# Kernel optimization log

Measured on AMD Instinct MI355X. Metric: run time of the kernel, lower is better.

## Reference

```python
import jax, jax.numpy as jnp
from jax import lax
import numpy as np

NB_CODE = 16384
DIM = 128
SCALES = [(1, 1), (2, 2), (4, 4), (8, 8), (16, 16)]
PHI_IDX = [0, 1, 1, 2, 3]  # PhiPartiallyShared: argmin(|ticks - si/(SN-1)|), K=4, SN=5
RESI = 0.5  # abs(quant_resi)
BETA = 0.25


def _cubic(x, a=-0.75):
    # PyTorch bicubic kernel (cubic convolution, a=-0.75)
    ax = np.abs(x)
    return np.where(ax <= 1.0, (a + 2.0) * ax ** 3 - (a + 3.0) * ax ** 2 + 1.0,
                    np.where(ax < 2.0, a * ax ** 3 - 5.0 * a * ax ** 2 + 8.0 * a * ax - 4.0 * a, 0.0))


def bicubic_mat(n_in, n_out):
    # 1D interpolation matrix matching torch F.interpolate(mode='bicubic', align_corners=False)
    W = np.zeros((n_out, n_in), dtype=np.float32)
    scale = n_in / n_out
    for i in range(n_out):
        x = (i + 0.5) * scale - 0.5
        x0 = int(np.floor(x))
        t = x - x0
        for k in range(4):
            idx = min(max(x0 - 1 + k, 0), n_in - 1)  # border clamp
            W[i, idx] += _cubic(t + 1.0 - k)
    return jnp.asarray(W)


def phi_apply(h, w, b):
    y = lax.conv_general_dilated(h, w, (1, 1), 'SAME',
                                 dimension_numbers=('NCHW', 'OIHW', 'NCHW'))
    y = y + b[None, :, None, None]
    return h * (1.0 - RESI) + y * RESI


def setup_inputs() -> dict:
    key = jax.random.key(0)
    k1, k2, k3, k4 = jax.random.split(key, 4)
    B, C, J, L = 16, DIM, 16, 16
    f_bcjl = jax.random.normal(k1, (B, C, J, L), dtype=jnp.float32)
    emb = jax.random.normal(k2, (NB_CODE, C), dtype=jnp.float32) * 0.02
    # 4 partially-shared Phi convs (3x3, C->C)
    phi_w = jax.random.normal(k3, (4, C, C, 3, 3), dtype=jnp.float32) * (1.0 / np.sqrt(C * 9))
    phi_b = jax.random.normal(k4, (4, C), dtype=jnp.float32) * 0.01
    return {'f_bcjl': f_bcjl, 'emb': emb, 'phi_w': phi_w, 'phi_b': phi_b}


def reference(f_bcjl, emb, phi_w, phi_b):
    B, C, J, L = f_bcjl.shape
    SN = len(SCALES)
    f_ng = lax.stop_gradient(f_bcjl)
    f_rest = f_ng
    f_hat = jnp.zeros_like(f_ng)
    loss = jnp.float32(0.0)
    e_sq = jnp.sum(emb * emb, axis=1)  # [K]
    idx_all = []
    for si, (sn, tn) in enumerate(SCALES):
        if si != SN - 1:
            # 'area' downsample == integer-factor average pooling here
            r = f_rest.reshape(B, C, sn, J // sn, tn, L // tn).mean(axis=(3, 5))
        else:
            r = f_rest
        rNC = r.transpose(0, 2, 3, 1).reshape(-1, C)  # [N, C]
        d = jnp.sum(rNC * rNC, axis=1, keepdims=True) + e_sq - 2.0 * (rNC @ emb.T)
        idx = jnp.argmin(d, axis=1)  # [N]
        idx_all.append(idx)
        h = emb[idx].reshape(B, sn, tn, C).transpose(0, 3, 1, 2)  # [B,C,sn,tn]
        if si != SN - 1:
            Wj = bicubic_mat(sn, J)
            Wl = bicubic_mat(tn, L)
            h = jnp.einsum('js,bcst,lt->bcjl', Wj, h, Wl)
        k = PHI_IDX[si]
        h = phi_apply(h, phi_w[k], phi_b[k])
        f_hat = f_hat + h
        f_rest = f_rest - h
        loss = loss + BETA * jnp.mean((lax.stop_gradient(f_hat) - f_bcjl) ** 2) \
                    + jnp.mean((f_hat - f_ng) ** 2)
    loss = loss / SN
    idx_cat = jnp.concatenate(idx_all)
    counts = jnp.zeros((NB_CODE,), jnp.float32).at[idx_cat].add(1.0)
    p = counts / idx_cat.shape[0]
    perplexity = jnp.exp(-jnp.sum(p * jnp.log(p + 1e-10)))
    # straight-through estimator
    f_hat_out = lax.stop_gradient(f_hat) - f_ng + f_bcjl
    return (f_hat_out, loss, perplexity)
```

## Files before the change

kernel.cpp:

```cpp
#include <hip/hip_runtime.h>
#include <hip/hip_bf16.h>
#include <math.h>

#define BATCH 16
#define CDIM  128
#define NCODE 16384
#define ELEMS 524288
#define NTOT  5456
#define WEXT_TOT 589824
#define LOSS_COEF 4.76837158203125e-7f

typedef __attribute__((ext_vector_type(8))) short short8;
typedef __attribute__((ext_vector_type(4))) float float4v;
typedef unsigned short ushortT;
typedef unsigned long long u64;
typedef unsigned int u32;

__device__ __forceinline__ ushortT f2bf(float x) {
    __hip_bfloat16 h = __float2bfloat16(x);
    return *reinterpret_cast<ushortT*>(&h);
}
__device__ __forceinline__ float bf2f(ushortT b) {
    __hip_bfloat16 h = *reinterpret_cast<__hip_bfloat16*>(&b);
    return __bfloat162float(h);
}
__device__ __forceinline__ u32 ford(float v) {
    u32 b = __float_as_uint(v);
    return b ^ ((u32)((int)b >> 31) | 0x80000000u);
}

__device__ double cubic_d(double x) {
    const double a = -0.75;
    double ax = fabs(x);
    if (ax <= 1.0) return (a + 2.0) * ax * ax * ax - (a + 3.0) * ax * ax + 1.0;
    if (ax < 2.0)  return a * ax * ax * ax - 5.0 * a * ax * ax + 8.0 * a * ax - 4.0 * a;
    return 0.0;
}

__global__ __launch_bounds__(256)
void k_prologue(const float* __restrict__ f, const float* __restrict__ emb,
                const float* __restrict__ phi_w,
                float* __restrict__ f_rest, float* __restrict__ f_hat,
                float* __restrict__ esq, ushortT* __restrict__ embext,
                ushortT* __restrict__ wext, float* __restrict__ wmat,
                float* __restrict__ lossA) {
    const int t = threadIdx.x;
    const int id = blockIdx.x * 256 + t;

    if (id < ELEMS) {
        f_rest[id] = f[id];
        f_hat[id] = 0.f;
        int row = id >> 5, c4 = id & 31;
        float4 v = reinterpret_cast<const float4*>(emb + (size_t)row * CDIM)[c4];
        float xs[4] = {v.x, v.y, v.z, v.w};
        ushortT hi[4], lo[4];
        float ss = 0.f;
        #pragma unroll
        for (int i = 0; i < 4; ++i) {
            hi[i] = f2bf(xs[i]);
            lo[i] = f2bf(xs[i] - bf2f(hi[i]));
            ss += xs[i] * xs[i];
        }
        ushortT* base = embext + (size_t)row * 256;
        *reinterpret_cast<ushort4*>(base + c4 * 4)       = make_ushort4(hi[0], hi[1], hi[2], hi[3]);
        *reinterpret_cast<ushort4*>(base + 128 + c4 * 4) = make_ushort4(lo[0], lo[1], lo[2], lo[3]);
        #pragma unroll
        for (int off = 16; off; off >>= 1) ss += __shfl_down(ss, off);
        if ((t & 31) == 0) esq[row] = ss;
    }
    if (id < WEXT_TOT) {
        int k4 = id / 147456, rem = id % 147456;
        int co = rem / 1152, kk = rem % 1152;
        int off = kk >> 7, ci = kk & 127;
        float v = 0.5f * phi_w[(((size_t)(k4 * 128 + co)) * 128 + ci) * 9 + off];
        if (ci == co && off == 4) v += 0.5f;
        wext[id] = f2bf(v);
    }
    if (blockIdx.x == 0 && t < 64) {
        int sIdx = t >> 4;
        int S = 1 << sIdx;
        int j = t & 15;
        const int offs[4] = {0, 16, 48, 112};
        double row[8];
        for (int s = 0; s < 8; ++s) row[s] = 0.0;
        double scale = (double)S / 16.0;
        double x = (j + 0.5) * scale - 0.5;
        double x0 = floor(x);
        double tt = x - x0;
        for (int k = 0; k < 4; ++k) {
            int idx = (int)x0 - 1 + k;
            idx = idx < 0 ? 0 : (idx > S - 1 ? S - 1 : idx);
            row[idx] += cubic_d(tt + 1.0 - k);
        }
        for (int s = 0; s < S; ++s) wmat[offs[sIdx] + j * S + s] = (float)row[s];
    }
    if (id == 0) lossA[0] = 0.f;
}

__global__ __launch_bounds__(256)
void k_packext(const float* __restrict__ fr, ushortT* __restrict__ re,
               u64* __restrict__ packed, int N, int padN, int S, int lgS) {
    int id = blockIdx.x * 256 + threadIdx.x;
    if (id < N) packed[id] = ~0ull;
    if (id >= padN * 32) return;
    int row = id >> 5, c4 = id & 31;
    ushortT hi[4], lo[4];
    if (row < N) {
        int mask = S - 1;
        int tt = row & mask, ssi = (row >> lgS) & mask, b = row >> (2 * lgS);
        int bs = 16 >> lgS;
        float inv = 1.f / (float)(bs * bs);
        #pragma unroll
        for (int u = 0; u < 4; ++u) {
            int c = c4 * 4 + u;
            const float* base = fr + (size_t)(b * 128 + c) * 256 + (ssi * bs) * 16 + tt * bs;
            float acc = 0.f;
            for (int jj = 0; jj < bs; ++jj)
                for (int ll = 0; ll < bs; ++ll)
                    acc += base[jj * 16 + ll];
            float x = acc * inv;
            hi[u] = f2bf(x);
            lo[u] = f2bf(x - bf2f(hi[u]));
        }
    } else {
        #pragma unroll
        for (int u = 0; u < 4; ++u) { hi[u] = 0; lo[u] = 0; }
    }
    ushortT* base = re + (size_t)row * 256;
    *reinterpret_cast<ushort4*>(base + c4 * 4)       = make_ushort4(hi[0], hi[1], hi[2], hi[3]);
    *reinterpret_cast<ushort4*>(base + 128 + c4 * 4) = make_ushort4(lo[0], lo[1], lo[2], lo[3]);
}

__global__ __launch_bounds__(256)
void k_packext_wave(const float* __restrict__ fr, ushortT* __restrict__ re,
                    u64* __restrict__ packed, int N, int padN, int S, int lgS) {
    int gid = blockIdx.x * 256 + threadIdx.x;
    int wid = gid >> 6, lane = threadIdx.x & 63;
    if (wid >= padN * 128) return;
    int row = wid >> 7, c = wid & 127;
    float x = 0.f;
    if (row < N) {
        int mask = S - 1;
        int tt = row & mask, ssi = (row >> lgS) & mask, b = row >> (2 * lgS);
        int lgbs = 4 - lgS, bs = 1 << lgbs, cnt = bs * bs;
        const float* base = fr + (size_t)(b * 128 + c) * 256 + (ssi * bs) * 16 + tt * bs;
        float acc = 0.f;
        for (int e = lane; e < cnt; e += 64)
            acc += base[(e >> lgbs) * 16 + (e & (bs - 1))];
        #pragma unroll
        for (int off = 32; off; off >>= 1) acc += __shfl_down(acc, off);
        x = acc / (float)cnt;
    }
    if (lane == 0) {
        ushortT h = f2bf(x);
        re[(size_t)row * 256 + c] = h;
        re[(size_t)row * 256 + 128 + c] = f2bf(x - bf2f(h));
        if (c == 0 && row < N) packed[row] = ~0ull;
    }
}

template<int TI>
__global__ __launch_bounds__(256)
void k_argmin_mfma(const ushortT* __restrict__ rext, const ushortT* __restrict__ embext,
                   const float* __restrict__ esq, int N, int kPerSplit,
                   u64* __restrict__ packed) {
    __shared__ ushortT Btile[2][64 * 32 * 8];
    const int t = threadIdx.x;
    const int w = t >> 6;
    const int lane = t & 63;
    const int ln = lane & 15;
    const int q  = lane >> 4;
    const int k0beg = blockIdx.y * kPerSplit;
    const int rowW = blockIdx.x * (64 * TI) + w * (16 * TI);

    short8 a[TI][8];
    #pragma unroll
    for (int ti = 0; ti < TI; ++ti) {
        const ushortT* r0 = rext + (size_t)(rowW + ti * 16 + ln) * 256 + q * 8;
        #pragma unroll
        for (int sb = 0; sb < 8; ++sb)
            a[ti][sb] = *reinterpret_cast<const short8*>(r0 + sb * 32);
    }

    float minv[TI][4];
    int   mini[TI][4];
    #pragma unroll
    for (int ti = 0; ti < TI; ++ti)
        #pragma unroll
        for (int rg = 0; rg < 4; ++rg) { minv[ti][rg] = 3.4e38f; mini[ti][rg] = 0; }

    const int tiles = kPerSplit >> 6;

    #pragma unroll
    for (int i = 0; i < 8; ++i) {
        int F = (i * 4 + w) * 64 + lane;
        int n = F >> 5, cs = F & 31;
        int cp = (cs & ~7) | ((cs & 7) ^ (n & 7));
        const ushortT* src = embext + (size_t)(k0beg + n) * 256 + cp * 8;
        __builtin_amdgcn_global_load_lds(
            (const __attribute__((address_space(1))) unsigned int*)src,
            (__attribute__((address_space(3))) unsigned int*)&Btile[0][(size_t)((i * 4 + w) * 64) * 8],
            16, 0, 0);
    }

    for (int it = 0; it < tiles; ++it) {
        __syncthreads();
        if (it + 1 < tiles) {
            int k1 = k0beg + (it + 1) * 64;
            int bu = (it + 1) & 1;
            #pragma unroll
            for (int i = 0; i < 8; ++i) {
                int F = (i * 4 + w) * 64 + lane;
                int n = F >> 5, cs = F & 31;
                int cp = (cs & ~7) | ((cs & 7) ^ (n & 7));
                const ushortT* src = embext + (size_t)(k1 + n) * 256 + cp * 8;
                __builtin_amdgcn_global_load_lds(
                    (const __attribute__((address_space(1))) unsigned int*)src,
                    (__attribute__((address_space(3))) unsigned int*)&Btile[bu][(size_t)((i * 4 + w) * 64) * 8],
                    16, 0, 0);
            }
        }
        const ushortT* Bt = Btile[it & 1];
        const int k0 = k0beg + it * 64;

        #pragma unroll
        for (int sub = 0; sub < 4; ++sub) {
            int n = sub * 16 + ln;
            short8 bfr[8];
            #pragma unroll
            for (int sb = 0; sb < 8; ++sb) {
                int cp = q + 4 * sb;
                int cs = (cp & ~7) | ((cp & 7) ^ (n & 7));
                bfr[sb] = *reinterpret_cast<const short8*>(&Bt[(size_t)(n * 32 + cs) * 8]);
            }
            float4v acc[TI];
            #pragma unroll
            for (int ti = 0; ti < TI; ++ti) acc[ti] = (float4v){0.f, 0.f, 0.f, 0.f};
            #pragma unroll
            for (int s = 0; s < 12; ++s) {
                int as = s < 8 ? s : s - 8;
                int bs = s < 4 ? s : s - 4;
                #pragma unroll
                for (int ti = 0; ti < TI; ++ti)
                    acc[ti] = __builtin_amdgcn_mfma_f32_16x16x32_bf16(a[ti][as], bfr[bs], acc[ti], 0, 0, 0);
            }
            int kc = k0 + sub * 16 + ln;
            float es = esq[kc];
            #pragma unroll
            for (int ti = 0; ti < TI; ++ti)
                #pragma unroll
                for (int rg = 0; rg < 4; ++rg) {
                    float sc = fmaf(-2.f, acc[ti][rg], es);
                    if (sc < minv[ti][rg]) { minv[ti][rg] = sc; mini[ti][rg] = kc; }
                }
        }
    }

    #pragma unroll
    for (int ti = 0; ti < TI; ++ti)
        #pragma unroll
        for (int rg = 0; rg < 4; ++rg) {
            float v = minv[ti][rg]; int ix = mini[ti][rg];
            #pragma unroll
            for (int off = 1; off < 16; off <<= 1) {
                float ov = __shfl_xor(v, off);
                int   oi = __shfl_xor(ix, off);
                if (ov < v || (ov == v && oi < ix)) { v = ov; ix = oi; }
            }
            if (ln == 0) {
                int row = rowW + ti * 16 + q * 4 + rg;
                if (row < N) {
                    u64 p = ((u64)ford(v) << 32) | (u32)ix;
                    atomicMin(&packed[row], p);
                }
            }
        }
}

__global__ __launch_bounds__(256)
void k_upconv(const float* __restrict__ emb, const u64* __restrict__ packed,
              const float* __restrict__ wm, int S, int lastScale,
              const ushortT* __restrict__ wext, const float* __restrict__ bias,
              const float* __restrict__ f_in, float* __restrict__ f_hat,
              float* __restrict__ f_rest, float* __restrict__ loss_acc) {
    __shared__ __align__(16) ushortT Htile[3 * 16 * 128];
    __shared__ __align__(16) float tmpS[3 * 8 * 128];
    __shared__ float wsum[4];
    const int t = threadIdx.x;
    const int b = blockIdx.x >> 4;
    const int j = blockIdx.x & 15;
    const int l = t >> 4, c8 = t & 15;
    const int phys = (c8 & 8) | ((c8 & 7) ^ (l & 7));

    if (lastScale) {
        #pragma unroll
        for (int r = 0; r < 3; ++r) {
            int jin = j - 1 + r;
            float acc[8] = {0.f, 0.f, 0.f, 0.f, 0.f, 0.f, 0.f, 0.f};
            if (jin >= 0 && jin < 16) {
                int idx = (int)(u32)(packed[(b * 16 + jin) * 16 + l] & 0xFFFFFFFFull);
                const float* er = emb + (size_t)idx * CDIM + c8 * 8;
                float4 e0 = *reinterpret_cast<const float4*>(er);
                float4 e1 = *reinterpret_cast<const float4*>(er + 4);
                acc[0] = e0.x; acc[1] = e0.y; acc[2] = e0.z; acc[3] = e0.w;
                acc[4] = e1.x; acc[5] = e1.y; acc[6] = e1.z; acc[7] = e1.w;
            }
            short8 o;
            #pragma unroll
            for (int i = 0; i < 8; ++i) o[i] = (short)f2bf(acc[i]);
            *reinterpret_cast<short8*>(&Htile[((size_t)(r * 16 + l) * 16 + phys) * 8]) = o;
        }
    } else {
        int items = 3 * S * 16;
        for (int i = t; i < items; i += 256) {
            int r = i / (S * 16);
            int rem = i - r * (S * 16);
            int t2 = rem >> 4, cc8 = rem & 15;
            int jin = j - 1 + r;
            float a0[8] = {0.f, 0.f, 0.f, 0.f, 0.f, 0.f, 0.f, 0.f};
            if (jin >= 0 && jin < 16) {
                for (int s = 0; s < S; ++s) {
                    float wjv = wm[jin * S + s];
                    int idx = (int)(u32)(packed[b * S * S + s * S + t2] & 0xFFFFFFFFull);
                    const float* er = emb + (size_t)idx * CDIM + cc8 * 8;
                    float4 e0 = *reinterpret_cast<const float4*>(er);
                    float4 e1 = *reinterpret_cast<const float4*>(er + 4);
                    a0[0] += wjv * e0.x; a0[1] += wjv * e0.y;
                    a0[2] += wjv * e0.z; a0[3] += wjv * e0.w;
                    a0[4] += wjv * e1.x; a0[5] += wjv * e1.y;
                    a0[6] += wjv * e1.z; a0[7] += wjv * e1.w;
                }
            }
            float* tp = &tmpS[((size_t)(r * 8 + t2)) * 128 + cc8 * 8];
            *reinterpret_cast<float4*>(tp)     = make_float4(a0[0], a0[1], a0[2], a0[3]);
            *reinterpret_cast<float4*>(tp + 4) = make_float4(a0[4], a0[5], a0[6], a0[7]);
        }
        __syncthreads();
        #pragma unroll
        for (int r = 0; r < 3; ++r) {
            float acc[8] = {0.f, 0.f, 0.f, 0.f, 0.f, 0.f, 0.f, 0.f};
            for (int t2 = 0; t2 < S; ++t2) {
                float wlv = wm[l * S + t2];
                const float* tp = &tmpS[((size_t)(r * 8 + t2)) * 128 + c8 * 8];
                float4 v0 = *reinterpret_cast<const float4*>(tp);
                float4 v1 = *reinterpret_cast<const float4*>(tp + 4);
                acc[0] += wlv * v0.x; acc[1] += wlv * v0.y;
                acc[2] += wlv * v0.z; acc[3] += wlv * v0.w;
                acc[4] += wlv * v1.x; acc[5] += wlv * v1.y;
                acc[6] += wlv * v1.z; acc[7] += wlv * v1.w;
            }
            short8 o;
            #pragma unroll
            for (int i = 0; i < 8; ++i) o[i] = (short)f2bf(acc[i]);
            *reinterpret_cast<short8*>(&Htile[((size_t)(r * 16 + l) * 16 + phys) * 8]) = o;
        }
    }
    __syncthreads();

    const int w = t >> 6, lane = t & 63;
    const int ln = lane & 15, q = lane >> 4;
    const int co0 = w * 32;
    const ushortT* wA = wext + (size_t)(co0 + ln) * 1152;
    float4v acc2[2] = {{0.f, 0.f, 0.f, 0.f}, {0.f, 0.f, 0.f, 0.f}};
    const short8 zz = {0, 0, 0, 0, 0, 0, 0, 0};

    #pragma unroll 3
    for (int off = 0; off < 9; ++off) {
        const int dj = off / 3, dl = off % 3;
        int cIn = ln + dl - 1;
        int cCl = cIn < 0 ? 0 : (cIn > 15 ? 15 : cIn);
        bool oob = (cIn != cCl);
        int rb = (dj * 16 + cCl) * 128;
        #pragma unroll
        for (int g = 0; g < 4; ++g) {
            int csl = g * 4 + q;
            int ph2 = (csl & 8) | ((csl & 7) ^ (cCl & 7));
            short8 av = *reinterpret_cast<const short8*>(&Htile[rb + ph2 * 8]);
            if (oob) av = zz;
            const ushortT* wr = wA + (off * 4 + g) * 32 + q * 8;
            short8 b0 = *reinterpret_cast<const short8*>(wr);
            short8 b1 = *reinterpret_cast<const short8*>(wr + 16 * 1152);
            acc2[0] = __builtin_amdgcn_mfma_f32_16x16x32_bf16(av, b0, acc2[0], 0, 0, 0);
            acc2[1] = __builtin_amdgcn_mfma_f32_16x16x32_bf16(av, b1, acc2[1], 0, 0, 0);
        }
    }

    float s = 0.f;
    #pragma unroll
    for (int sn = 0; sn < 2; ++sn) {
        int co = co0 + sn * 16 + ln;
        float bsv = 0.5f * bias[co];
        size_t gi = ((size_t)(b * 128 + co) * 16 + j) * 16 + q * 4;
        float4 fh = *reinterpret_cast<const float4*>(&f_hat[gi]);
        float4 fr = *reinterpret_cast<const float4*>(&f_rest[gi]);
        float4 fv = *reinterpret_cast<const float4*>(&f_in[gi]);
        float o0 = acc2[sn][0] + bsv, o1 = acc2[sn][1] + bsv;
        float o2 = acc2[sn][2] + bsv, o3 = acc2[sn][3] + bsv;
        fh.x += o0; fh.y += o1; fh.z += o2; fh.w += o3;
        fr.x -= o0; fr.y -= o1; fr.z -= o2; fr.w -= o3;
        *reinterpret_cast<float4*>(&f_hat[gi]) = fh;
        *reinterpret_cast<float4*>(&f_rest[gi]) = fr;
        float d0 = fh.x - fv.x, d1 = fh.y - fv.y;
        float d2 = fh.z - fv.z, d3 = fh.w - fv.w;
        s += d0 * d0 + d1 * d1 + d2 * d2 + d3 * d3;
    }
    #pragma unroll
    for (int off = 32; off; off >>= 1) s += __shfl_down(s, off);
    if (lane == 0) wsum[w] = s;
    __syncthreads();
    if (t == 0)
        atomicAdd(loss_acc, (wsum[0] + wsum[1] + wsum[2] + wsum[3]) * LOSS_COEF);
}

__global__ __launch_bounds__(256)
void k_final(const u64* __restrict__ packed, const float* __restrict__ loss_acc,
             float* __restrict__ out) {
    __shared__ u32 cnt2[NCODE / 2];
    __shared__ float ws4[4];
    int t = threadIdx.x;
    for (int i = t; i < NCODE / 2; i += 256) cnt2[i] = 0;
    __syncthreads();
    for (int i = t; i < NTOT; i += 256) {
        int idx = (int)(u32)(packed[i] & 0xFFFFFFFFull);
        atomicAdd(&cnt2[idx >> 1], (idx & 1) ? 65536u : 1u);
    }
    __syncthreads();
    float s = 0.f;
    for (int k = t; k < NCODE; k += 256) {
        u32 c = cnt2[k >> 1];
        c = (k & 1) ? (c >> 16) : (c & 0xFFFFu);
        float p = (float)c * (1.0f / (float)NTOT);
        s += p * logf(p + 1e-10f);
    }
    #pragma unroll
    for (int off = 32; off; off >>= 1) s += __shfl_down(s, off);
    if ((t & 63) == 0) ws4[t >> 6] = s;
    __syncthreads();
    if (t == 0) {
        out[ELEMS]     = loss_acc[0];
        out[ELEMS + 1] = expf(-(ws4[0] + ws4[1] + ws4[2] + ws4[3]));
    }
}

extern "C" void kernel_launch(void* const* d_in, const int* in_sizes, int n_in,
                              void* d_out, int out_size, void* d_ws, size_t ws_size,
                              hipStream_t stream) {
    const float* f     = (const float*)d_in[0];
    const float* emb   = (const float*)d_in[1];
    const float* phi_w = (const float*)d_in[2];
    const float* phi_b = (const float*)d_in[3];
    float* out = (float*)d_out;

    float* wsf = (float*)d_ws;
    float*   f_rest = wsf;
    float*   esq    = wsf + 524288;
    float*   wmat   = wsf + 540672;
    float*   lossA  = wsf + 540928;
    u64*     packed = (u64*)(wsf + 540992);
    ushortT* embext = (ushortT*)(wsf + 557376);
    ushortT* rext   = (ushortT*)(wsf + 2654528);
    ushortT* wext   = (ushortT*)(wsf + 3178816);

    k_prologue<<<2304, 256, 0, stream>>>(f, emb, phi_w, f_rest, out, esq,
                                         embext, wext, wmat, lossA);

    const int Ss[5]     = {1, 2, 4, 8, 16};
    const int lgSs[5]   = {0, 1, 2, 3, 4};
    const int phiIdx[5] = {0, 1, 1, 2, 3};
    const int ksplit[5] = {256, 256, 128, 64, 32};
    const int TIa[5]    = {2, 2, 2, 2, 4};
    const int wmOff[5]  = {0, 16, 48, 112, 0};
    const int pOff[5]   = {0, 16, 80, 336, 1360};

    for (int si = 0; si < 5; ++si) {
        int S = Ss[si], lgS = lgSs[si];
        int N = 16 * S * S;
        int TI = TIa[si];
        int align = 64 * TI;
        int padN = (N + align - 1) & ~(align - 1);
        u64* pk = packed + pOff[si];

        if (S <= 2)
            k_packext_wave<<<padN * 128 / 4, 256, 0, stream>>>(f_rest, rext, pk, N, padN, S, lgS);
        else
            k_packext<<<padN * 32 / 256, 256, 0, stream>>>(f_rest, rext, pk, N, padN, S, lgS);

        int KS = ksplit[si];
        if (TI == 2)
            k_argmin_mfma<2><<<dim3(padN / 128, KS), 256, 0, stream>>>(rext, embext, esq,
                                                                       N, NCODE / KS, pk);
        else
            k_argmin_mfma<4><<<dim3(padN / 256, KS), 256, 0, stream>>>(rext, embext, esq,
                                                                       N, NCODE / KS, pk);

        int k = phiIdx[si];
        k_upconv<<<256, 256, 0, stream>>>(emb, pk, wmat + wmOff[si], S, si == 4 ? 1 : 0,
                                          wext + (size_t)k * 147456,
                                          phi_b + (size_t)k * 128, f, out, f_rest, lossA);
    }

    k_final<<<1, 256, 0, stream>>>(packed, lossA, out);
}
```

Before: 341.6 us.

## Fuse scale-0 packing into prologue and read f_rest directly in final argmin

Scale 0's mean-pool and hi/lo bf16 split now happen inside the prologue kernel, which also zero-pads the packed rows and initialises all packed argmin slots. That removes the packext launch for scales 0 and 4. The final scale's argmin kernel now loads f_rest straight from global memory and splits it to bf16 in registers. Scale 3 moves to the 4-tile argmin variant with a different k-split, adding launch bounds for two blocks per SM. The direct loads are strided by 256 floats per channel, so they may be less efficient than the packed layout they replace.

Measured after the change: 357.9 us. +4.8%, slower.

```diff
diff --git a/kernel.cpp b/kernel.cpp
--- a/kernel.cpp
+++ b/kernel.cpp
@@ -43,12 +43,16 @@
                 float* __restrict__ f_rest, float* __restrict__ f_hat,
                 float* __restrict__ esq, ushortT* __restrict__ embext,
                 ushortT* __restrict__ wext, float* __restrict__ wmat,
-                float* __restrict__ lossA) {
+                float* __restrict__ lossA, ushortT* __restrict__ rext,
+                u64* __restrict__ packed) {
+    __shared__ float red[4];
     const int t = threadIdx.x;
-    const int id = blockIdx.x * 256 + t;
-
-    if (id < ELEMS) {
-        f_rest[id] = f[id];
+    const int bid = blockIdx.x;
+    const int id = bid * 256 + t;
+
+    if (bid < 2048) {
+        float fv = f[id];
+        f_rest[id] = fv;
         f_hat[id] = 0.f;
         int row = id >> 5, c4 = id & 31;
         float4 v = reinterpret_cast<const float4*>(emb + (size_t)row * CDIM)[c4];
@@ -67,6 +71,23 @@
         #pragma unroll
         for (int off = 16; off; off >>= 1) ss += __shfl_down(ss, off);
         if ((t & 31) == 0) esq[row] = ss;
+
+        float s = fv;
+        #pragma unroll
+        for (int off = 32; off; off >>= 1) s += __shfl_down(s, off);
+        if ((t & 63) == 0) red[t >> 6] = s;
+        __syncthreads();
+        if (t == 0) {
+            float m = (red[0] + red[1] + red[2] + red[3]) * (1.f / 256.f);
+            int b = bid >> 7, c = bid & 127;
+            ushortT h = f2bf(m);
+            rext[b * 256 + c] = h;
+            rext[b * 256 + 128 + c] = f2bf(m - bf2f(h));
+        }
+    } else {
+        int idz = (bid - 2048) * 256 + t;
+        if (idz < 30720)
+            reinterpret_cast<u32*>(rext + 16 * 256)[idz] = 0;
     }
     if (id < WEXT_TOT) {
         int k4 = id / 147456, rem = id % 147456;
@@ -76,7 +97,7 @@
         if (ci == co && off == 4) v += 0.5f;
         wext[id] = f2bf(v);
     }
-    if (blockIdx.x == 0 && t < 64) {
+    if (bid == 0 && t < 64) {
         int sIdx = t >> 4;
         int S = 1 << sIdx;
         int j = t & 15;
@@ -95,6 +116,7 @@
         for (int s = 0; s < S; ++s) wmat[offs[sIdx] + j * S + s] = (float)row[s];
     }
     if (id == 0) lossA[0] = 0.f;
+    if (id < 8192) packed[id] = ~0ull;
 }
 
 __global__ __launch_bounds__(256)
@@ -159,11 +181,10 @@
     }
 }
 
-template<int TI>
 __global__ __launch_bounds__(256)
-void k_argmin_mfma(const ushortT* __restrict__ rext, const ushortT* __restrict__ embext,
-                   const float* __restrict__ esq, int N, int kPerSplit,
-                   u64* __restrict__ packed) {
+void k_argmin_mfma2(const ushortT* __restrict__ rext, const ushortT* __restrict__ embext,
+                    const float* __restrict__ esq, int N, int kPerSplit,
+                    u64* __restrict__ packed) {
     __shared__ ushortT Btile[2][64 * 32 * 8];
     const int t = threadIdx.x;
     const int w = t >> 6;
@@ -171,21 +192,21 @@
     const int ln = lane & 15;
     const int q  = lane >> 4;
     const int k0beg = blockIdx.y * kPerSplit;
-    const int rowW = blockIdx.x * (64 * TI) + w * (16 * TI);
-
-    short8 a[TI][8];
-    #pragma unroll
-    for (int ti = 0; ti < TI; ++ti) {
+    const int rowW = blockIdx.x * 128 + w * 32;
+
+    short8 a[2][8];
+    #pragma unroll
+    for (int ti = 0; ti < 2; ++ti) {
         const ushortT* r0 = rext + (size_t)(rowW + ti * 16 + ln) * 256 + q * 8;
         #pragma unroll
         for (int sb = 0; sb < 8; ++sb)
             a[ti][sb] = *reinterpret_cast<const short8*>(r0 + sb * 32);
     }
 
-    float minv[TI][4];
-    int   mini[TI][4];
-    #pragma unroll
-    for (int ti = 0; ti < TI; ++ti)
+    float minv[2][4];
+    int   mini[2][4];
+    #pragma unroll
+    for (int ti = 0; ti < 2; ++ti)
         #pragma unroll
         for (int rg = 0; rg < 4; ++rg) { minv[ti][rg] = 3.4e38f; mini[ti][rg] = 0; }
 
@@ -233,21 +254,21 @@
                 int cs = (cp & ~7) | ((cp & 7) ^ (n & 7));
                 bfr[sb] = *reinterpret_cast<const short8*>(&Bt[(size_t)(n * 32 + cs) * 8]);
             }
-            float4v acc[TI];
-            #pragma unroll
-            for (int ti = 0; ti < TI; ++ti) acc[ti] = (float4v){0.f, 0.f, 0.f, 0.f};
+            float4v acc[2];
+            #pragma unroll
+            for (int ti = 0; ti < 2; ++ti) acc[ti] = (float4v){0.f, 0.f, 0.f, 0.f};
             #pragma unroll
             for (int s = 0; s < 12; ++s) {
                 int as = s < 8 ? s : s - 8;
                 int bs = s < 4 ? s : s - 4;
                 #pragma unroll
-                for (int ti = 0; ti < TI; ++ti)
+                for (int ti = 0; ti < 2; ++ti)
                     acc[ti] = __builtin_amdgcn_mfma_f32_16x16x32_bf16(a[ti][as], bfr[bs], acc[ti], 0, 0, 0);
             }
             int kc = k0 + sub * 16 + ln;
             float es = esq[kc];
             #pragma unroll
-            for (int ti = 0; ti < TI; ++ti)
+            for (int ti = 0; ti < 2; ++ti)
                 #pragma unroll
                 for (int rg = 0; rg < 4; ++rg) {
                     float sc = fmaf(-2.f, acc[ti][rg], es);
@@ -257,7 +278,144 @@
     }
 
     #pragma unroll
-    for (int ti = 0; ti < TI; ++ti)
+    for (int ti = 0; ti < 2; ++ti)
+        #pragma unroll
+        for (int rg = 0; rg < 4; ++rg) {
+            float v = minv[ti][rg]; int ix = mini[ti][rg];
+            #pragma unroll
+            for (int off = 1; off < 16; off <<= 1) {
+                float ov = __shfl_xor(v, off);
+                int   oi = __shfl_xor(ix, off);
+                if (ov < v || (ov == v && oi < ix)) { v = ov; ix = oi; }
+            }
+            if (ln == 0) {
+                int row = rowW + ti * 16 + q * 4 + rg;
+                if (row < N) {
+                    u64 p = ((u64)ford(v) << 32) | (u32)ix;
+                    atomicMin(&packed[row], p);
+                }
+            }
+        }
+}
+
+__global__ __launch_bounds__(256, 2)
+void k_argmin_mfma4(const ushortT* __restrict__ rext, const float* __restrict__ f_rest,
+                    const ushortT* __restrict__ embext, const float* __restrict__ esq,
+                    int N, int kPerSplit, int direct, u64* __restrict__ packed) {
+    __shared__ ushortT Btile[2][64 * 32 * 8];
+    const int t = threadIdx.x;
+    const int w = t >> 6;
+    const int lane = t & 63;
+    const int ln = lane & 15;
+    const int q  = lane >> 4;
+    const int k0beg = blockIdx.y * kPerSplit;
+    const int rowW = blockIdx.x * 256 + w * 64;
+
+    short8 a[4][8];
+    if (direct) {
+        #pragma unroll
+        for (int ti = 0; ti < 4; ++ti) {
+            int row = rowW + ti * 16 + ln;
+            int b = row >> 8, pos = row & 255;
+            const float* base = f_rest + (size_t)(b * 128) * 256 + pos;
+            #pragma unroll
+            for (int sb = 0; sb < 4; ++sb) {
+                int c0 = (q + 4 * sb) * 8;
+                #pragma unroll
+                for (int u = 0; u < 8; ++u) {
+                    float x = base[(size_t)(c0 + u) * 256];
+                    ushortT hv = f2bf(x);
+                    a[ti][sb][u] = (short)hv;
+                    a[ti][sb + 4][u] = (short)f2bf(x - bf2f(hv));
+                }
+            }
+        }
+    } else {
+        #pragma unroll
+        for (int ti = 0; ti < 4; ++ti) {
+            const ushortT* r0 = rext + (size_t)(rowW + ti * 16 + ln) * 256 + q * 8;
+            #pragma unroll
+            for (int sb = 0; sb < 8; ++sb)
+                a[ti][sb] = *reinterpret_cast<const short8*>(r0 + sb * 32);
+        }
+    }
+
+    float minv[4][4];
+    int   mini[4][4];
+    #pragma unroll
+    for (int ti = 0; ti < 4; ++ti)
+        #pragma unroll
+        for (int rg = 0; rg < 4; ++rg) { minv[ti][rg] = 3.4e38f; mini[ti][rg] = 0; }
+
+    const int tiles = kPerSplit >> 6;
+
+    #pragma unroll
+    for (int i = 0; i < 8; ++i) {
+        int F = (i * 4 + w) * 64 + lane;
+        int n = F >> 5, cs = F & 31;
+        int cp = (cs & ~7) | ((cs & 7) ^ (n & 7));
+        const ushortT* src = embext + (size_t)(k0beg + n) * 256 + cp * 8;
+        __builtin_amdgcn_global_load_lds(
+            (const __attribute__((address_space(1))) unsigned int*)src,
+            (__attribute__((address_space(3))) unsigned int*)&Btile[0][(size_t)((i * 4 + w) * 64) * 8],
+            16, 0, 0);
+    }
+
+    for (int it = 0; it < tiles; ++it) {
+        __syncthreads();
+        if (it + 1 < tiles) {
+            int k1 = k0beg + (it + 1) * 64;
+            int bu = (it + 1) & 1;
+            #pragma unroll
+            for (int i = 0; i < 8; ++i) {
+                int F = (i * 4 + w) * 64 + lane;
+                int n = F >> 5, cs = F & 31;
+                int cp = (cs & ~7) | ((cs & 7) ^ (n & 7));
+                const ushortT* src = embext + (size_t)(k1 + n) * 256 + cp * 8;
+                __builtin_amdgcn_global_load_lds(
+                    (const __attribute__((address_space(1))) unsigned int*)src,
+                    (__attribute__((address_space(3))) unsigned int*)&Btile[bu][(size_t)((i * 4 + w) * 64) * 8],
+                    16, 0, 0);
+            }
+        }
+        const ushortT* Bt = Btile[it & 1];
+        const int k0 = k0beg + it * 64;
+
+        #pragma unroll
+        for (int sub = 0; sub < 4; ++sub) {
+            int n = sub * 16 + ln;
+            short8 bfr[8];
+            #pragma unroll
+            for (int sb = 0; sb < 8; ++sb) {
+                int cp = q + 4 * sb;
+                int cs = (cp & ~7) | ((cp & 7) ^ (n & 7));
+                bfr[sb] = *reinterpret_cast<const short8*>(&Bt[(size_t)(n * 32 + cs) * 8]);
+            }
+            float4v acc[4];
+            #pragma unroll
+            for (int ti = 0; ti < 4; ++ti) acc[ti] = (float4v){0.f, 0.f, 0.f, 0.f};
+            #pragma unroll
+            for (int s = 0; s < 12; ++s) {
+                int as = s < 8 ? s : s - 8;
+                int bs = s < 4 ? s : s - 4;
+                #pragma unroll
+                for (int ti = 0; ti < 4; ++ti)
+                    acc[ti] = __builtin_amdgcn_mfma_f32_16x16x32_bf16(a[ti][as], bfr[bs], acc[ti], 0, 0, 0);
+            }
+            int kc = k0 + sub * 16 + ln;
+            float es = esq[kc];
+            #pragma unroll
+            for (int ti = 0; ti < 4; ++ti)
+                #pragma unroll
+                for (int rg = 0; rg < 4; ++rg) {
+                    float sc = fmaf(-2.f, acc[ti][rg], es);
+                    if (sc < minv[ti][rg]) { minv[ti][rg] = sc; mini[ti][rg] = kc; }
+                }
+        }
+    }
+
+    #pragma unroll
+    for (int ti = 0; ti < 4; ++ti)
         #pragma unroll
         for (int rg = 0; rg < 4; ++rg) {
             float v = minv[ti][rg]; int ix = mini[ti][rg];
@@ -462,36 +620,40 @@
     ushortT* wext   = (ushortT*)(wsf + 3178816);
 
     k_prologue<<<2304, 256, 0, stream>>>(f, emb, phi_w, f_rest, out, esq,
-                                         embext, wext, wmat, lossA);
+                                         embext, wext, wmat, lossA, rext, packed);
 
     const int Ss[5]     = {1, 2, 4, 8, 16};
     const int lgSs[5]   = {0, 1, 2, 3, 4};
     const int phiIdx[5] = {0, 1, 1, 2, 3};
-    const int ksplit[5] = {256, 256, 128, 64, 32};
-    const int TIa[5]    = {2, 2, 2, 2, 4};
     const int wmOff[5]  = {0, 16, 48, 112, 0};
     const int pOff[5]   = {0, 16, 80, 336, 1360};
 
     for (int si = 0; si < 5; ++si) {
         int S = Ss[si], lgS = lgSs[si];
         int N = 16 * S * S;
-        int TI = TIa[si];
-        int align = 64 * TI;
-        int padN = (N + align - 1) & ~(align - 1);
         u64* pk = packed + pOff[si];
 
-        if (S <= 2)
+        if (si == 1) {
+            int padN = 128;
             k_packext_wave<<<padN * 128 / 4, 256, 0, stream>>>(f_rest, rext, pk, N, padN, S, lgS);
-        else
+        } else if (si == 2 || si == 3) {
+            int padN = (N + 127) & ~127;
             k_packext<<<padN * 32 / 256, 256, 0, stream>>>(f_rest, rext, pk, N, padN, S, lgS);
-
-        int KS = ksplit[si];
-        if (TI == 2)
-            k_argmin_mfma<2><<<dim3(padN / 128, KS), 256, 0, stream>>>(rext, embext, esq,
-                                                                       N, NCODE / KS, pk);
-        else
-            k_argmin_mfma<4><<<dim3(padN / 256, KS), 256, 0, stream>>>(rext, embext, esq,
-                                                                       N, NCODE / KS, pk);
+        }
+
+        if (si <= 2) {
+            const int KSs[3] = {256, 256, 128};
+            int KS = KSs[si];
+            int padN = (N + 127) & ~127;
+            k_argmin_mfma2<<<dim3(padN / 128, KS), 256, 0, stream>>>(rext, embext, esq,
+                                                                     N, NCODE / KS, pk);
+        } else if (si == 3) {
+            k_argmin_mfma4<<<dim3(4, 128), 256, 0, stream>>>(rext, f_rest, embext, esq,
+                                                             N, NCODE / 128, 0, pk);
+        } else {
+            k_argmin_mfma4<<<dim3(16, 32), 256, 0, stream>>>(rext, f_rest, embext, esq,
+                                                             N, NCODE / 32, 1, pk);
+        }
 
         int k = phiIdx[si];
         k_upconv<<<256, 256, 0, stream>>>(emb, pk, wmat + wmOff[si], S, si == 4 ? 1 : 0,
```
